# Optimization experiments

Measured on AMD Instinct MI355X. Metric: run time of the kernel, lower is better.

Reference implementation:

```python
import jax, jax.numpy as jnp
import numpy as np

EPS = 1e-6


def _mp_match(reps, att, kernel):
    """BiMPM multi-perspective match.
    reps: (B,L,D); att: (B,L,D) or (B,1,D); kernel: (M,D).
    Returns (B,L,1+M): [tanh(sum(reps*att)), tanh(sum_d reps*kernel_m*att)].
    """
    prod = reps * att                                   # (B,L,D)
    cos = jnp.tanh(jnp.sum(prod, axis=-1, keepdims=True))   # (B,L,1)
    mp = jnp.tanh(jnp.einsum('bld,md->blm', prod, kernel))  # (B,L,M)
    return jnp.concatenate([cos, mp], axis=-1)


def setup_inputs() -> dict:
    key = jax.random.key(0)
    ks = jax.random.split(key, 12)
    B, Llt, Lrt, D, M, A = 32, 128, 128, 512, 64, 128
    H = D // 2
    u = lambda k, shape: jax.random.uniform(k, shape, jnp.float32, -0.05, 0.05)  # keras 'uniform' init
    return {
        'reps_lt': jax.random.normal(ks[0], (B, Llt, D), jnp.float32),
        'h_lt_fw': jax.random.normal(ks[1], (B, H), jnp.float32),
        'h_lt_bw': jax.random.normal(ks[2], (B, H), jnp.float32),
        'reps_rt': jax.random.normal(ks[3], (B, Lrt, D), jnp.float32),
        'h_rt_fw': jax.random.normal(ks[4], (B, H), jnp.float32),
        'h_rt_bw': jax.random.normal(ks[5], (B, H), jnp.float32),
        'kernel_full': u(ks[6], (M, D)),
        'kernel_mpool': u(ks[7], (M, D)),
        'attn_w1': u(ks[8], (D, A)),
        'diag_w': u(ks[9], (A,)),
        'kernel_att': u(ks[10], (M, D)),
        'kernel_maxatt': u(ks[11], (M, D)),
    }


def reference(reps_lt, h_lt_fw, h_lt_bw, reps_rt, h_rt_fw, h_rt_bw,
              kernel_full, kernel_mpool, attn_w1, diag_w,
              kernel_att, kernel_maxatt):
    # ---- full match: each left timestep vs last BiLSTM state of right ----
    h_rt = jnp.concatenate([h_rt_fw, h_rt_bw], axis=-1)[:, None, :]  # (B,1,D)
    full = _mp_match(reps_lt, h_rt, kernel_full)                     # (B,Ll,1+M)

    # ---- max-pooling match ----
    # t[b,r,l,m] = tanh(sum_d R[b,r,d]*K[m,d]*L[b,l,d]); max over right positions r
    r_scaled = jnp.einsum('brd,md->brmd', reps_rt, kernel_mpool)     # (B,Lr,M,D)
    t = jnp.tanh(jnp.einsum('brmd,bld->brlm', r_scaled, reps_lt))    # (B,Lr,Ll,M)
    mpool = jnp.max(t, axis=1)                                       # (B,Ll,M)

    # ---- attentive match ----
    a_lt = jnp.tanh(reps_lt @ attn_w1) * diag_w                      # (B,Ll,A)
    a_rt = jnp.tanh(reps_rt @ attn_w1)                               # (B,Lr,A)
    scores = jnp.einsum('bla,bra->blr', a_lt, a_rt)                  # (B,Ll,Lr)
    probs = jax.nn.softmax(scores, axis=-1)
    att = jnp.einsum('blr,brd->bld', probs, reps_rt)                 # (B,Ll,D)
    attentive = _mp_match(reps_lt, att, kernel_att)                  # (B,Ll,1+M)

    # ---- max-attentive match ----
    num = jnp.einsum('bld,brd->blr', reps_lt, reps_rt)
    n_lt = jnp.sqrt(jnp.maximum(jnp.sum(reps_lt * reps_lt, -1), EPS))[:, :, None]
    n_rt = jnp.sqrt(jnp.maximum(jnp.sum(reps_rt * reps_rt, -1), EPS))[:, None, :]
    rel = num / n_rt / n_lt                                          # (B,Ll,Lr)
    idx = jnp.argmax(rel, axis=2)                                    # (B,Ll) int
    max_att = jnp.take_along_axis(reps_rt, idx[:, :, None], axis=1)  # (B,Ll,D)
    maxatt = _mp_match(reps_lt, max_att, kernel_maxatt)              # (B,Ll,1+M)

    return jnp.concatenate([full, mpool, attentive, maxatt], axis=-1)  # (B,Ll,3+4M)
```

## Files before the change

kernel.cpp:

```cpp
#include <hip/hip_runtime.h>
#include <hip/hip_bf16.h>
#include <math.h>
#include <stdint.h>

typedef __attribute__((ext_vector_type(8))) short short8;
typedef __attribute__((ext_vector_type(4))) float float4v;

#define DEV static __device__ __forceinline__

DEV float bflo(unsigned int u) { union { unsigned int i; float f; } v; v.i = u << 16; return v.f; }
DEV float bfhi(unsigned int u) { union { unsigned int i; float f; } v; v.i = u & 0xffff0000u; return v.f; }
DEV unsigned short f2bf(float f) {
    union { float f; unsigned int i; } v; v.f = f;
    unsigned int x = v.i;
    return (unsigned short)((x + 0x7fffu + ((x >> 16) & 1u)) >> 16);
}
DEV unsigned int pack2(float a, float b) { return (unsigned int)f2bf(a) | ((unsigned int)f2bf(b) << 16); }
#if __has_builtin(__builtin_amdgcn_cvt_pk_bf16_f32)
DEV unsigned int pack2_fast(float a, float b) {
    typedef __attribute__((ext_vector_type(2))) short short2v;
    short2v r = __builtin_amdgcn_cvt_pk_bf16_f32(a, b);
    union { short2v s; unsigned int u; } v; v.s = r; return v.u;
}
#else
DEV unsigned int pack2_fast(float a, float b) { return pack2(a, b); }
#endif
DEV void unpack8(uint4 u, float* f) {
    f[0]=bflo(u.x); f[1]=bfhi(u.x); f[2]=bflo(u.y); f[3]=bfhi(u.y);
    f[4]=bflo(u.z); f[5]=bfhi(u.z); f[6]=bflo(u.w); f[7]=bfhi(u.w);
}

DEV void async16(const unsigned short* g, unsigned short* l) {
    __builtin_amdgcn_global_load_lds(
        (const __attribute__((address_space(1))) unsigned int*)g,
        (__attribute__((address_space(3))) unsigned int*)l, 16, 0, 0);
}

__global__ __launch_bounds__(256) void prep_kernel(const float* __restrict__ lt,
                                                   const float* __restrict__ rt,
                                                   const float* __restrict__ kf,
                                                   const float* __restrict__ kmp,
                                                   const float* __restrict__ ka,
                                                   const float* __restrict__ km,
                                                   const float* __restrict__ w1,
                                                   unsigned short* __restrict__ ltb,
                                                   unsigned short* __restrict__ rtb,
                                                   unsigned short* __restrict__ kb,
                                                   unsigned short* __restrict__ w1t,
                                                   unsigned short* __restrict__ rtbT,
                                                   double* __restrict__ rsq) {
    __shared__ double ws2[2][2];
    __shared__ float tile[32][33];
    int bid = blockIdx.x, t = threadIdx.x;
    if (bid < 1024) {
        bool isRt = bid >= 512;
        int base = (isRt ? (bid - 512) : bid) * 8;
        int rl = t >> 7;
        int c  = t & 127;
        const float* srcb = isRt ? rt : lt;
        unsigned short* dstb = isRt ? rtb : ltb;
        #pragma unroll
        for (int p = 0; p < 4; ++p) {
            int row = base + p * 2 + rl;
            const float* src = srcb + (size_t)row * 512;
            float4 v = *(const float4*)(src + c * 4);
            ushort4 o;
            o.x = f2bf(v.x); o.y = f2bf(v.y); o.z = f2bf(v.z); o.w = f2bf(v.w);
            *(ushort4*)(dstb + (size_t)row * 512 + c * 4) = o;
            if (isRt) {
                double s = (double)v.x * v.x + (double)v.y * v.y
                         + (double)v.z * v.z + (double)v.w * v.w;
                #pragma unroll
                for (int off = 1; off < 64; off <<= 1) s += __shfl_xor(s, off, 64);
                if ((c & 63) == 0) ws2[rl][c >> 6] = s;
                __syncthreads();
                if (c == 0) rsq[row] = 1.0 / sqrt(ws2[rl][0] + ws2[rl][1]);
                __syncthreads();
            }
        }
    } else if (bid < 1152) {
        int kbk = bid - 1024;
        int ksel = kbk >> 5;
        const float* src = (ksel == 0) ? kf : (ksel == 1) ? kmp : (ksel == 2) ? ka : km;
        int off = (kbk & 31) * 1024 + t * 4;
        float4 v = *(const float4*)(src + off);
        ushort4 o;
        o.x = f2bf(v.x); o.y = f2bf(v.y); o.z = f2bf(v.z); o.w = f2bf(v.w);
        *(ushort4*)(kb + ksel * 32768 + off) = o;
    } else if (bid < 1216) {
        int b2 = bid - 1152;
        int d0 = (b2 & 15) * 32, a0 = (b2 >> 4) * 32;
        int r = t >> 5, c = t & 31;
        #pragma unroll
        for (int i = 0; i < 32; i += 8)
            tile[r + i][c] = w1[(size_t)(d0 + r + i) * 128 + a0 + c];
        __syncthreads();
        #pragma unroll
        for (int i = 0; i < 32; i += 8)
            w1t[(size_t)(a0 + r + i) * 512 + d0 + c] = f2bf(tile[c][r + i]);
    } else {
        int b3 = bid - 1216;
        int b = b3 >> 6;
        int tid = b3 & 63;
        int d0 = (tid & 15) * 32;
        int r0 = (tid >> 4) * 32;
        int r = t >> 5, c = t & 31;
        #pragma unroll
        for (int i = 0; i < 32; i += 8)
            tile[r + i][c] = rt[(size_t)(b * 128 + r0 + r + i) * 512 + d0 + c];
        __syncthreads();
        #pragma unroll
        for (int i = 0; i < 32; i += 8)
            rtbT[(size_t)(b * 512 + d0 + r + i) * 128 + r0 + c] = f2bf(tile[c][r + i]);
    }
}

__global__ __launch_bounds__(256, 3) void mid_kernel(
        const unsigned short* __restrict__ ltb,
        const unsigned short* __restrict__ rtb,
        const unsigned short* __restrict__ w1t,
        const float* __restrict__ diag,
        unsigned short* __restrict__ a_all,
        const double* __restrict__ rsq,
        unsigned int* __restrict__ candp) {
    __shared__ __align__(16) unsigned char smem[52224];
    int bx = blockIdx.x;
    int t = threadIdx.x;
    int wave = t >> 6, lane = t & 63;
    int q = lane >> 4, col = lane & 15, kq = q * 8;

    if (bx < 32) {
        int sb = bx;
        int xcd = sb & 7;
        int b = xcd * 4 + (sb >> 3);
        unsigned short* ltS = (unsigned short*)smem;
        unsigned short* rtL = (unsigned short*)(smem + 16384);
        float* rsqf = (float*)(smem + 49152);
        unsigned int (*candL)[2] = (unsigned int(*)[2])(smem + 49664);
        int wl = wave & 1, wr = wave >> 1;
        const unsigned short* ltp = ltb + (size_t)b * 65536;
        const unsigned short* rtp = rtb + (size_t)b * 65536;
        int srow = t >> 3, cg8 = t & 7, cg = cg8 * 8;
        int gsw = (cg8 ^ (srow & 7)) * 8;
        int wbase = (t & ~63) * 8;

        #pragma unroll
        for (int it = 0; it < 4; ++it)
            async16(rtp + (size_t)(it * 32 + srow) * 512 + gsw,
                    rtL + it * 2048 + wbase);
        uint4 plt[4];
        #pragma unroll
        for (int it = 0; it < 4; ++it)
            plt[it] = *(const uint4*)(ltp + (size_t)(it * 32 + srow) * 512 + cg);
        if (t < 128) rsqf[t] = (float)rsq[b * 128 + t];

        float4v acc[4][4] = {};
        for (int k0i = 0; k0i < 8; ++k0i) {
            #pragma unroll
            for (int it = 0; it < 4; ++it) {
                int row = it * 32 + srow;
                *(uint4*)&ltS[row * 64 + gsw] = plt[it];
            }
            __syncthreads();
            if (k0i < 7) {
                int k0n = (k0i + 1) * 64;
                int bofs = ((k0i + 1) & 1) * 8192;
                #pragma unroll
                for (int it = 0; it < 4; ++it)
                    async16(rtp + (size_t)(it * 32 + srow) * 512 + k0n + gsw,
                            rtL + bofs + it * 2048 + wbase);
                #pragma unroll
                for (int it = 0; it < 4; ++it)
                    plt[it] = *(const uint4*)(ltp + (size_t)(it * 32 + srow) * 512 + k0n + cg);
            }
            const unsigned short* rb = rtL + (k0i & 1) * 8192;
            #pragma unroll
            for (int kk = 0; kk < 64; kk += 32) {
                short8 af[4], bfr[4];
                #pragma unroll
                for (int i = 0; i < 4; ++i) {
                    int rowA = wl * 64 + i * 16 + col;
                    int slotA = ((kk >> 3) + q) ^ (rowA & 7);
                    af[i] = *(const short8*)&ltS[rowA * 64 + slotA * 8];
                }
                #pragma unroll
                for (int j = 0; j < 4; ++j) {
                    int row = wr * 64 + j * 16 + col;
                    int slot = ((kk >> 3) + q) ^ (row & 7);
                    bfr[j] = *(const short8*)&rb[row * 64 + slot * 8];
                }
                #pragma unroll
                for (int i = 0; i < 4; ++i)
                    #pragma unroll
                    for (int j = 0; j < 4; ++j)
                        acc[i][j] = __builtin_amdgcn_mfma_f32_16x16x32_bf16(af[i], bfr[j], acc[i][j], 0, 0, 0);
            }
            __syncthreads();
        }
        float rq[4];
        #pragma unroll
        for (int j = 0; j < 4; ++j) rq[j] = rsqf[wr * 64 + j * 16 + col];
        #pragma unroll
        for (int i = 0; i < 4; ++i)
            #pragma unroll
            for (int ii = 0; ii < 4; ++ii) {
                float v1 = -3.0e38f, v2 = -3.0e38f; int i1 = 0, i2 = 1;
                #pragma unroll
                for (int j = 0; j < 4; ++j) {
                    int rc = wr * 64 + j * 16 + col;
                    float s = acc[i][j][ii] * rq[j];
                    if (s > v1) { v2 = v1; i2 = i1; v1 = s; i1 = rc; }
                    else if (s > v2) { v2 = s; i2 = rc; }
                }
                #pragma unroll
                for (int off = 1; off < 16; off <<= 1) {
                    float u1 = __shfl_xor(v1, off, 64); int j1 = __shfl_xor(i1, off, 64);
                    float u2 = __shfl_xor(v2, off, 64); int j2 = __shfl_xor(i2, off, 64);
                    if (u1 > v1) {
                        float ov = v1; int oi = i1;
                        v1 = u1; i1 = j1;
                        if (u2 > ov) { v2 = u2; i2 = j2; } else { v2 = ov; i2 = oi; }
                    } else if (u1 > v2) { v2 = u1; i2 = j1; }
                }
                if (col == 0)
                    candL[wl * 64 + i * 16 + q * 4 + ii][wr] =
                        (unsigned int)i1 | ((unsigned int)i2 << 8);
            }
        __syncthreads();
        if (t < 128)
            candp[b * 128 + t] = candL[t][0] | (candL[t][1] << 16);

    } else {
        int R0 = (bx - 32) * 32;
        unsigned short (*aS)[72] = (unsigned short(*)[72])smem;
        unsigned short (*bS)[72] = (unsigned short(*)[72])(smem + 4608);
        float* diagS = (float*)(smem + 4608 + 18432);
        int wl = wave & 1, wr = wave >> 1;
        if (t < 128) diagS[t] = diag[t];
        const unsigned short* src = (R0 < 4096) ? (ltb + (size_t)R0 * 512) : (rtb + (size_t)(R0 - 4096) * 512);
        float4v acc[4] = {};
        for (int k0 = 0; k0 < 512; k0 += 64) {
            {
                int row = t >> 3, cg = (t & 7) * 8;
                *(uint4*)&aS[row][cg] = *(const uint4*)(src + (size_t)row * 512 + k0 + cg);
            }
            #pragma unroll
            for (int it = 0; it < 4; ++it) {
                int id = it * 256 + t;
                int row = id >> 3, cg = (id & 7) * 8;
                *(uint4*)&bS[row][cg] = *(const uint4*)(w1t + (size_t)row * 512 + k0 + cg);
            }
            __syncthreads();
            #pragma unroll
            for (int kk = 0; kk < 64; kk += 32) {
                short8 af = *(const short8*)&aS[wl * 16 + col][kk + kq];
                #pragma unroll
                for (int j = 0; j < 4; ++j) {
                    short8 bf = *(const short8*)&bS[wr * 64 + j * 16 + col][kk + kq];
                    acc[j] = __builtin_amdgcn_mfma_f32_16x16x32_bf16(af, bf, acc[j], 0, 0, 0);
                }
            }
            __syncthreads();
        }
        bool isLt = (R0 < 4096);
        #pragma unroll
        for (int j = 0; j < 4; ++j)
            #pragma unroll
            for (int ii = 0; ii < 4; ++ii) {
                int rowl = wl * 16 + q * 4 + ii;
                int n = wr * 64 + j * 16 + col;
                float v = tanhf(acc[j][ii]);
                if (isLt) v *= diagS[n];
                a_all[((size_t)(R0 + rowl)) * 128 + n] = f2bf(v);
            }
    }
}

__global__ __launch_bounds__(512, 4) void main_kernel(
        const unsigned short* __restrict__ ltb,
        const unsigned short* __restrict__ rtb,
        const unsigned short* __restrict__ kmb,
        const unsigned short* __restrict__ a_all,
        const unsigned short* __restrict__ rtbT,
        const float* __restrict__ ltf,
        const float* __restrict__ rtf,
        const double* __restrict__ rsq,
        const unsigned short* __restrict__ kb,
        const float* __restrict__ hfw,
        const float* __restrict__ hbw,
        const unsigned int* __restrict__ candp,
        float* __restrict__ out) {
    __shared__ __align__(16) unsigned char smem[81664];
    int bx = blockIdx.x;
    int t = threadIdx.x;
    int wave = t >> 6, lane = t & 63;
    int q = lane >> 4, col = lane & 15, kq = q * 8;

    int xcd = bx & 7;
    int s = bx >> 3;
    int g = s / 11;
    int r = s - g * 11;

    if (r < 8) {
        int lm = g * 8 + r;
        int b = xcd * 4 + (lm >> 6);
        int m = lm & 63;
        unsigned short* ltS = (unsigned short*)smem;
        unsigned short* rtL = (unsigned short*)(smem + 16384);
        float (*mx)[4] = (float(*)[4])(smem + 49152);
        int wl = wave & 1, wr = wave >> 1;
        const unsigned short* ltp = ltb + (size_t)b * 65536;
        const unsigned short* rtp = rtb + (size_t)b * 65536;
        const unsigned short* kr = kmb + (size_t)m * 512;
        int srow = t >> 3, cg8 = t & 7, cg = cg8 * 8;
        int gsw = (cg8 ^ (srow & 7)) * 8;

        #pragma unroll
        for (int it = 0; it < 2; ++it)
            async16(rtp + (size_t)(it * 64 + srow) * 512 + gsw,
                    rtL + it * 4096 + t * 8);
        uint4 pk = *(const uint4*)(kr + cg);
        uint4 plt[2];
        #pragma unroll
        for (int it = 0; it < 2; ++it)
            plt[it] = *(const uint4*)(ltp + (size_t)(it * 64 + srow) * 512 + cg);

        float4v acc[4][2] = {};
        for (int k0i = 0; k0i < 8; ++k0i) {
            float kf8[8]; unpack8(pk, kf8);
            #pragma unroll
            for (int it = 0; it < 2; ++it) {
                int row = it * 64 + srow;
                float lf[8]; unpack8(plt[it], lf);
                uint4 sv;
                sv.x = pack2_fast(lf[0] * kf8[0], lf[1] * kf8[1]);
                sv.y = pack2_fast(lf[2] * kf8[2], lf[3] * kf8[3]);
                sv.z = pack2_fast(lf[4] * kf8[4], lf[5] * kf8[5]);
                sv.w = pack2_fast(lf[6] * kf8[6], lf[7] * kf8[7]);
                *(uint4*)&ltS[row * 64 + gsw] = sv;
            }
            __syncthreads();
            if (k0i < 7) {
                int k0n = (k0i + 1) * 64;
                int bofs = ((k0i + 1) & 1) * 8192;
                #pragma unroll
                for (int it = 0; it < 2; ++it)
                    async16(rtp + (size_t)(it * 64 + srow) * 512 + k0n + gsw,
                            rtL + bofs + it * 4096 + t * 8);
                pk = *(const uint4*)(kr + k0n + cg);
                #pragma unroll
                for (int it = 0; it < 2; ++it)
                    plt[it] = *(const uint4*)(ltp + (size_t)(it * 64 + srow) * 512 + k0n + cg);
            }
            const unsigned short* rb = rtL + (k0i & 1) * 8192;
            #pragma unroll
            for (int kk = 0; kk < 64; kk += 32) {
                short8 af[4], bfr[2];
                #pragma unroll
                for (int i = 0; i < 4; ++i) {
                    int rowA = wl * 64 + i * 16 + col;
                    int slotA = ((kk >> 3) + q) ^ (rowA & 7);
                    af[i] = *(const short8*)&ltS[rowA * 64 + slotA * 8];
                }
                #pragma unroll
                for (int j = 0; j < 2; ++j) {
                    int row = wr * 32 + j * 16 + col;
                    int slot = ((kk >> 3) + q) ^ (row & 7);
                    bfr[j] = *(const short8*)&rb[row * 64 + slot * 8];
                }
                #pragma unroll
                for (int i = 0; i < 4; ++i)
                    #pragma unroll
                    for (int j = 0; j < 2; ++j)
                        acc[i][j] = __builtin_amdgcn_mfma_f32_16x16x32_bf16(af[i], bfr[j], acc[i][j], 0, 0, 0);
            }
            __syncthreads();
        }
        #pragma unroll
        for (int i = 0; i < 4; ++i)
            #pragma unroll
            for (int ii = 0; ii < 4; ++ii) {
                float v = fmaxf(acc[i][0][ii], acc[i][1][ii]);
                #pragma unroll
                for (int off = 1; off < 16; off <<= 1) v = fmaxf(v, __shfl_xor(v, off, 64));
                if (col == 0) mx[wl * 64 + i * 16 + q * 4 + ii][wr] = v;
            }
        __syncthreads();
        if (t < 128) {
            float v = fmaxf(fmaxf(mx[t][0], mx[t][1]), fmaxf(mx[t][2], mx[t][3]));
            out[((size_t)(b * 128 + t)) * 259 + 65 + m] = tanhf(v);
        }

    } else if (r == 8) {
        int la = g;
        int b = xcd * 4 + (la >> 3);
        int lg = la & 7;
        int L0 = lg * 16;
        unsigned short (*altS)[136]  = (unsigned short(*)[136])(smem);
        unsigned short (*artS)[136]  = (unsigned short(*)[136])(smem + 4352);
        unsigned short (*prodsF)[520]= (unsigned short(*)[520])(smem + 55552);
        float (*pmax)[8] = (float(*)[8])(smem + 80640);
        float (*psum)[8] = (float(*)[8])(smem + 81152);
        const unsigned short* kb_att = kb + 2 * 32768;

        if (t < 256) {
            int row = t >> 4, c0 = (t & 15) * 8;
            *(uint4*)&altS[row][c0] = *(const uint4*)(a_all + ((size_t)(b * 128 + L0 + row)) * 128 + c0);
        }
        {
            int row = t >> 2, c0 = (t & 3) * 32;
            const unsigned short* src = a_all + ((size_t)(4096 + b * 128 + row)) * 128 + c0;
            #pragma unroll
            for (int i = 0; i < 4; ++i)
                *(uint4*)&artS[row][c0 + i * 8] = *(const uint4*)(src + i * 8);
        }
        __syncthreads();

        float4v acc = {};
        #pragma unroll
        for (int kk = 0; kk < 128; kk += 32) {
            short8 af = *(const short8*)&altS[col][kk + kq];
            short8 bf = *(const short8*)&artS[wave * 16 + col][kk + kq];
            acc = __builtin_amdgcn_mfma_f32_16x16x32_bf16(af, bf, acc, 0, 0, 0);
        }
        float m4[4], p4[4];
        #pragma unroll
        for (int ii = 0; ii < 4; ++ii) {
            float v = acc[ii];
            #pragma unroll
            for (int off = 1; off < 16; off <<= 1) v = fmaxf(v, __shfl_xor(v, off, 64));
            m4[ii] = v;
        }
        if (col == 0) {
            #pragma unroll
            for (int ii = 0; ii < 4; ++ii) pmax[q * 4 + ii][wave] = m4[ii];
        }
        __syncthreads();
        #pragma unroll
        for (int ii = 0; ii < 4; ++ii) {
            float M = pmax[q * 4 + ii][0];
            #pragma unroll
            for (int w = 1; w < 8; ++w) M = fmaxf(M, pmax[q * 4 + ii][w]);
            p4[ii] = expf(acc[ii] - M);
            float sv = p4[ii];
            #pragma unroll
            for (int off = 1; off < 16; off <<= 1) sv += __shfl_xor(sv, off, 64);
            m4[ii] = sv;
        }
        if (col == 0) {
            #pragma unroll
            for (int ii = 0; ii < 4; ++ii) psum[q * 4 + ii][wave] = m4[ii];
        }
        __syncthreads();
        unsigned short* Pb = (unsigned short*)smem;
        #pragma unroll
        for (int ii = 0; ii < 4; ++ii) {
            float S = psum[q * 4 + ii][0] + psum[q * 4 + ii][1] + psum[q * 4 + ii][2] + psum[q * 4 + ii][3]
                    + psum[q * 4 + ii][4] + psum[q * 4 + ii][5] + psum[q * 4 + ii][6] + psum[q * 4 + ii][7];
            Pb[(q * 4 + ii) * 136 + wave * 16 + col] = f2bf(p4[ii] / S);
        }

        unsigned short* Bc = (unsigned short*)(smem + 4352);
        float* attF = (float*)(smem + 39168);
        const unsigned short* rtT = rtbT + (size_t)b * 65536;
        for (int cc = 0; cc < 4; ++cc) {
            #pragma unroll
            for (int i = 0; i < 4; ++i) {
                int rid = i * 32 + (t >> 4);
                int d   = (rid >> 4) * 64 + cc * 16 + (rid & 15);
                int sg  = (t & 15) ^ (rid & 15);
                async16(rtT + (size_t)d * 128 + sg * 8, Bc + i * 4096 + t * 8);
            }
            __syncthreads();
            float4v pacc = {};
            #pragma unroll
            for (int ks = 0; ks < 4; ++ks) {
                short8 afP = *(const short8*)&Pb[col * 136 + ks * 32 + kq];
                short8 bfB = *(const short8*)&Bc[(wave * 16 + col) * 128 + (((ks * 4 + q) ^ col) * 8)];
                pacc = __builtin_amdgcn_mfma_f32_16x16x32_bf16(afP, bfB, pacc, 0, 0, 0);
            }
            #pragma unroll
            for (int ii = 0; ii < 4; ++ii)
                attF[(q * 4 + ii) * 512 + wave * 64 + cc * 16 + col] = pacc[ii];
            __syncthreads();
        }

        int l = t >> 5, cd = t & 31;
        float a8[2][8];
        #pragma unroll
        for (int pass = 0; pass < 2; ++pass) {
            *(float4*)&a8[pass][0] = *(const float4*)&attF[l * 512 + pass * 256 + cd * 8];
            *(float4*)&a8[pass][4] = *(const float4*)&attF[l * 512 + pass * 256 + cd * 8 + 4];
        }
        __syncthreads();

        int grow = b * 128 + L0 + l;
        const float* ltrow = ltf + (size_t)grow * 512;
        float csum = 0.f;
        #pragma unroll
        for (int pass = 0; pass < 2; ++pass) {
            int d0 = pass * 256 + cd * 8;
            float lf[8];
            *(float4*)&lf[0] = *(const float4*)(ltrow + d0);
            *(float4*)&lf[4] = *(const float4*)(ltrow + d0 + 4);
            float pf[8];
            #pragma unroll
            for (int k = 0; k < 8; ++k) { pf[k] = lf[k] * a8[pass][k]; csum += pf[k]; }
            uint4 o;
            o.x = pack2(pf[0], pf[1]); o.y = pack2(pf[2], pf[3]);
            o.z = pack2(pf[4], pf[5]); o.w = pack2(pf[6], pf[7]);
            *(uint4*)&prodsF[l][d0] = o;
        }
        #pragma unroll
        for (int off = 1; off < 32; off <<= 1) csum += __shfl_xor(csum, off, 64);
        if (cd == 0) out[(size_t)grow * 259 + 129] = tanhf(csum);

        unsigned short* Ks = &artS[0][0];
        float* red = (float*)(smem + 39168);
        for (int half = 0; half < 2; ++half) {
            __syncthreads();
            {
                int row = t >> 4, c0 = (t & 15) * 32;
                const unsigned short* src = kb_att + ((size_t)(half * 32 + row)) * 512 + c0;
                #pragma unroll
                for (int i = 0; i < 4; ++i)
                    *(uint4*)&Ks[row * 520 + c0 + i * 8] = *(const uint4*)(src + i * 8);
            }
            __syncthreads();
            float4v pacc[2] = {};
            #pragma unroll
            for (int kk = 0; kk < 64; kk += 32) {
                short8 af = *(const short8*)&prodsF[col][wave * 64 + kk + kq];
                #pragma unroll
                for (int j = 0; j < 2; ++j) {
                    short8 bf = *(const short8*)&Ks[(j * 16 + col) * 520 + wave * 64 + kk + kq];
                    pacc[j] = __builtin_amdgcn_mfma_f32_16x16x32_bf16(af, bf, pacc[j], 0, 0, 0);
                }
            }
            #pragma unroll
            for (int j = 0; j < 2; ++j)
                #pragma unroll
                for (int ii = 0; ii < 4; ++ii)
                    red[((wave * 2 + j) * 16 + q * 4 + ii) * 16 + col] = pacc[j][ii];
            __syncthreads();
            {
                int ll = t >> 5, jm = t & 31;
                int j = jm >> 4, mc = jm & 15;
                float sv = 0.f;
                #pragma unroll
                for (int w = 0; w < 8; ++w) sv += red[((w * 2 + j) * 16 + ll) * 16 + mc];
                out[((size_t)(b * 128 + L0 + ll)) * 259 + 130 + half * 32 + jm] = tanhf(sv);
            }
        }

    } else {
        int lb = g * 2 + (r - 9);
        int mode = (lb >> 5) ? 2 : 0;
        int b = xcd * 4 + ((lb >> 3) & 3);
        int lg = lb & 7;
        int L0 = lg * 16;
        unsigned short (*prods)[520] = (unsigned short(*)[520])smem;
        unsigned short* Ks = (unsigned short*)(smem + 16640);
        float* red = (float*)(smem + 49920);
        double* dvs2 = (double*)(smem + 66304);
        int* idxl = (int*)(smem + 66816);
        const unsigned short* Kp = kb + (size_t)((mode == 0) ? 0 : 3 * 32768);
        int obase = (mode == 0) ? 0 : 194;

        if (mode == 2) {
            int dotid = t >> 3, sub = t & 7;
            int l = dotid >> 2, c = dotid & 3;
            unsigned int cpl = candp[b * 128 + L0 + l];
            int rr0 = (cpl >> (c * 8)) & 0xff;
            const float* lrow = ltf + ((size_t)(b * 128 + L0 + l)) * 512;
            const float* rrow = rtf + ((size_t)(b * 128 + rr0)) * 512;
            double sv = 0.0;
            #pragma unroll 8
            for (int k = 0; k < 64; ++k) {
                int d = sub * 64 + k;
                sv = fma((double)lrow[d], (double)rrow[d], sv);
            }
            #pragma unroll
            for (int off = 1; off < 8; off <<= 1) sv += __shfl_xor(sv, off, 64);
            if (sub == 0) dvs2[dotid] = sv * rsq[b * 128 + rr0];
            __syncthreads();
            if (t < 16) {
                unsigned int cl = candp[b * 128 + L0 + t];
                int bi = 256; double bv = -1.0e300;
                #pragma unroll
                for (int cc = 0; cc < 4; ++cc) {
                    int rr = (cl >> (cc * 8)) & 0xff;
                    double v = dvs2[t * 4 + cc];
                    if (v > bv || (v == bv && rr < bi)) { bv = v; bi = rr; }
                }
                idxl[t] = bi;
            }
            __syncthreads();
        }

        if (t < 256) {
            int l = t >> 4, c = t & 15;
            int grow = b * 128 + L0 + l;
            const float* ltrow = ltf + (size_t)grow * 512;
            const unsigned short* avrow = 0;
            if (mode == 2) avrow = rtb + ((size_t)(b * 128 + idxl[l])) * 512;
            float csum = 0.f;
            #pragma unroll
            for (int pass = 0; pass < 4; ++pass) {
                int d0 = pass * 128 + c * 8;
                float lf[8], af[8], pf[8];
                *(float4*)&lf[0] = *(const float4*)(ltrow + d0);
                *(float4*)&lf[4] = *(const float4*)(ltrow + d0 + 4);
                if (mode == 0) {
                    const float* h = (d0 < 256) ? (hfw + b * 256 + d0) : (hbw + b * 256 + d0 - 256);
                    *(float4*)&af[0] = *(const float4*)h;
                    *(float4*)&af[4] = *(const float4*)(h + 4);
                } else {
                    uint4 av = *(const uint4*)(avrow + d0);
                    unpack8(av, af);
                }
                #pragma unroll
                for (int k = 0; k < 8; ++k) { pf[k] = lf[k] * af[k]; csum += pf[k]; }
                uint4 o;
                o.x = pack2(pf[0], pf[1]); o.y = pack2(pf[2], pf[3]);
                o.z = pack2(pf[4], pf[5]); o.w = pack2(pf[6], pf[7]);
                *(uint4*)&prods[l][d0] = o;
            }
            #pragma unroll
            for (int off = 1; off < 16; off <<= 1) csum += __shfl_xor(csum, off, 64);
            if (c == 0) out[(size_t)grow * 259 + obase] = tanhf(csum);
        }
        for (int half = 0; half < 2; ++half) {
            {
                int row = t >> 4, c0 = (t & 15) * 32;
                const unsigned short* src = Kp + ((size_t)(half * 32 + row)) * 512 + c0;
                #pragma unroll
                for (int i = 0; i < 4; ++i)
                    *(uint4*)&Ks[row * 520 + c0 + i * 8] = *(const uint4*)(src + i * 8);
            }
            __syncthreads();
            float4v acc2[2] = {};
            #pragma unroll
            for (int kk = 0; kk < 64; kk += 32) {
                short8 af = *(const short8*)&prods[col][wave * 64 + kk + kq];
                #pragma unroll
                for (int j = 0; j < 2; ++j) {
                    short8 bf = *(const short8*)&Ks[(j * 16 + col) * 520 + wave * 64 + kk + kq];
                    acc2[j] = __builtin_amdgcn_mfma_f32_16x16x32_bf16(af, bf, acc2[j], 0, 0, 0);
                }
            }
            #pragma unroll
            for (int j = 0; j < 2; ++j)
                #pragma unroll
                for (int ii = 0; ii < 4; ++ii)
                    red[((wave * 2 + j) * 16 + q * 4 + ii) * 16 + col] = acc2[j][ii];
            __syncthreads();
            {
                int ll = t >> 5, jm = t & 31;
                int j = jm >> 4, mc = jm & 15;
                float sv = 0.f;
                #pragma unroll
                for (int w = 0; w < 8; ++w) sv += red[((w * 2 + j) * 16 + ll) * 16 + mc];
                out[((size_t)(b * 128 + L0 + ll)) * 259 + obase + 1 + half * 32 + jm] = tanhf(sv);
            }
            __syncthreads();
        }
    }
}

extern "C" void kernel_launch(void* const* d_in, const int* in_sizes, int n_in,
                              void* d_out, int out_size, void* d_ws, size_t ws_size,
                              hipStream_t stream) {
    const float* lt  = (const float*)d_in[0];
    const float* rt  = (const float*)d_in[3];
    const float* hfw = (const float*)d_in[4];
    const float* hbw = (const float*)d_in[5];
    const float* kf  = (const float*)d_in[6];
    const float* kmp = (const float*)d_in[7];
    const float* w1  = (const float*)d_in[8];
    const float* dia = (const float*)d_in[9];
    const float* ka  = (const float*)d_in[10];
    const float* km  = (const float*)d_in[11];
    float* out = (float*)d_out;

    char* wsb = (char*)d_ws;
    unsigned short* ltb16 = (unsigned short*)(wsb);
    unsigned short* rtb16 = (unsigned short*)(wsb + 4194304);
    unsigned short* kb16  = (unsigned short*)(wsb + 8388608);
    unsigned short* w1t   = (unsigned short*)(wsb + 8650752);
    unsigned short* a_all = (unsigned short*)(wsb + 8781824);
    unsigned short* rtbT  = (unsigned short*)(wsb + 10878976);
    double*         rsq   = (double*)(wsb + 15073280);
    unsigned int*   candp = (unsigned int*)(wsb + 15106048);

    prep_kernel<<<3264, 256, 0, stream>>>(lt, rt, kf, kmp, ka, km, w1, ltb16, rtb16, kb16, w1t, rtbT, rsq);
    mid_kernel<<<288, 256, 0, stream>>>(ltb16, rtb16, w1t, dia, a_all, rsq, candp);
    main_kernel<<<2816, 512, 0, stream>>>(ltb16, rtb16, kb16 + 32768, a_all, rtbT,
                                          lt, rt, rsq, kb16, hfw, hbw, candp, out);
}
```

Measured before the change: 198.8 us.

## Merge prep and mid kernels, converting fp32 inputs to bf16 inline

Folds the mid kernel's work (max-attentive argmax candidate search and the attention projection tanh(X·W1)) into the prep kernel launch as extra blocks. These blocks now read fp32 inputs directly and convert to bf16 on the fly, instead of waiting for prep's bf16 copies. The right-side norms are computed inline in fp32, and W1 is read transposed straight from global memory, so the w1t transpose disappears. This removes one kernel launch and the serialization between prep and mid. The cost is more global traffic: fp32 loads, and uncoalesced strided W1 reads inside the MFMA loop. The candidate search also loses its async-load double buffering and now uses an fp32 norm where it used a double one.

New measurement: 195.0 us. About the same (-1.9%).

```diff
diff --git a/kernel.cpp b/kernel.cpp
--- a/kernel.cpp
+++ b/kernel.cpp
@@ -43,137 +43,64 @@
                                                    const float* __restrict__ ka,
                                                    const float* __restrict__ km,
                                                    const float* __restrict__ w1,
+                                                   const float* __restrict__ diag,
                                                    unsigned short* __restrict__ ltb,
                                                    unsigned short* __restrict__ rtb,
                                                    unsigned short* __restrict__ kb,
-                                                   unsigned short* __restrict__ w1t,
                                                    unsigned short* __restrict__ rtbT,
-                                                   double* __restrict__ rsq) {
-    __shared__ double ws2[2][2];
-    __shared__ float tile[32][33];
+                                                   double* __restrict__ rsq,
+                                                   unsigned short* __restrict__ a_all,
+                                                   unsigned int* __restrict__ candp) {
+    __shared__ __align__(16) unsigned char smem[34304];
     int bid = blockIdx.x, t = threadIdx.x;
-    if (bid < 1024) {
-        bool isRt = bid >= 512;
-        int base = (isRt ? (bid - 512) : bid) * 8;
-        int rl = t >> 7;
-        int c  = t & 127;
-        const float* srcb = isRt ? rt : lt;
-        unsigned short* dstb = isRt ? rtb : ltb;
-        #pragma unroll
-        for (int p = 0; p < 4; ++p) {
-            int row = base + p * 2 + rl;
-            const float* src = srcb + (size_t)row * 512;
-            float4 v = *(const float4*)(src + c * 4);
-            ushort4 o;
-            o.x = f2bf(v.x); o.y = f2bf(v.y); o.z = f2bf(v.z); o.w = f2bf(v.w);
-            *(ushort4*)(dstb + (size_t)row * 512 + c * 4) = o;
-            if (isRt) {
-                double s = (double)v.x * v.x + (double)v.y * v.y
-                         + (double)v.z * v.z + (double)v.w * v.w;
-                #pragma unroll
-                for (int off = 1; off < 64; off <<= 1) s += __shfl_xor(s, off, 64);
-                if ((c & 63) == 0) ws2[rl][c >> 6] = s;
-                __syncthreads();
-                if (c == 0) rsq[row] = 1.0 / sqrt(ws2[rl][0] + ws2[rl][1]);
-                __syncthreads();
-            }
-        }
-    } else if (bid < 1152) {
-        int kbk = bid - 1024;
-        int ksel = kbk >> 5;
-        const float* src = (ksel == 0) ? kf : (ksel == 1) ? kmp : (ksel == 2) ? ka : km;
-        int off = (kbk & 31) * 1024 + t * 4;
-        float4 v = *(const float4*)(src + off);
-        ushort4 o;
-        o.x = f2bf(v.x); o.y = f2bf(v.y); o.z = f2bf(v.z); o.w = f2bf(v.w);
-        *(ushort4*)(kb + ksel * 32768 + off) = o;
-    } else if (bid < 1216) {
-        int b2 = bid - 1152;
-        int d0 = (b2 & 15) * 32, a0 = (b2 >> 4) * 32;
-        int r = t >> 5, c = t & 31;
-        #pragma unroll
-        for (int i = 0; i < 32; i += 8)
-            tile[r + i][c] = w1[(size_t)(d0 + r + i) * 128 + a0 + c];
-        __syncthreads();
-        #pragma unroll
-        for (int i = 0; i < 32; i += 8)
-            w1t[(size_t)(a0 + r + i) * 512 + d0 + c] = f2bf(tile[c][r + i]);
-    } else {
-        int b3 = bid - 1216;
-        int b = b3 >> 6;
-        int tid = b3 & 63;
-        int d0 = (tid & 15) * 32;
-        int r0 = (tid >> 4) * 32;
-        int r = t >> 5, c = t & 31;
-        #pragma unroll
-        for (int i = 0; i < 32; i += 8)
-            tile[r + i][c] = rt[(size_t)(b * 128 + r0 + r + i) * 512 + d0 + c];
-        __syncthreads();
-        #pragma unroll
-        for (int i = 0; i < 32; i += 8)
-            rtbT[(size_t)(b * 512 + d0 + r + i) * 128 + r0 + c] = f2bf(tile[c][r + i]);
-    }
-}
-
-__global__ __launch_bounds__(256, 3) void mid_kernel(
-        const unsigned short* __restrict__ ltb,
-        const unsigned short* __restrict__ rtb,
-        const unsigned short* __restrict__ w1t,
-        const float* __restrict__ diag,
-        unsigned short* __restrict__ a_all,
-        const double* __restrict__ rsq,
-        unsigned int* __restrict__ candp) {
-    __shared__ __align__(16) unsigned char smem[52224];
-    int bx = blockIdx.x;
-    int t = threadIdx.x;
     int wave = t >> 6, lane = t & 63;
     int q = lane >> 4, col = lane & 15, kq = q * 8;
 
-    if (bx < 32) {
-        int sb = bx;
-        int xcd = sb & 7;
-        int b = xcd * 4 + (sb >> 3);
+    if (bid < 32) {
+        int xcd = bid & 7;
+        int b = xcd * 4 + (bid >> 3);
         unsigned short* ltS = (unsigned short*)smem;
-        unsigned short* rtL = (unsigned short*)(smem + 16384);
-        float* rsqf = (float*)(smem + 49152);
-        unsigned int (*candL)[2] = (unsigned int(*)[2])(smem + 49664);
+        unsigned short* rtS = (unsigned short*)(smem + 16384);
+        float* rnorm = (float*)(smem + 32768);
+        unsigned int (*candL)[2] = (unsigned int(*)[2])(smem + 33280);
         int wl = wave & 1, wr = wave >> 1;
-        const unsigned short* ltp = ltb + (size_t)b * 65536;
-        const unsigned short* rtp = rtb + (size_t)b * 65536;
+        const float* ltF = lt + (size_t)b * 65536;
+        const float* rtF = rt + (size_t)b * 65536;
         int srow = t >> 3, cg8 = t & 7, cg = cg8 * 8;
-        int gsw = (cg8 ^ (srow & 7)) * 8;
-        int wbase = (t & ~63) * 8;
-
-        #pragma unroll
-        for (int it = 0; it < 4; ++it)
-            async16(rtp + (size_t)(it * 32 + srow) * 512 + gsw,
-                    rtL + it * 2048 + wbase);
-        uint4 plt[4];
-        #pragma unroll
-        for (int it = 0; it < 4; ++it)
-            plt[it] = *(const uint4*)(ltp + (size_t)(it * 32 + srow) * 512 + cg);
-        if (t < 128) rsqf[t] = (float)rsq[b * 128 + t];
+        if (t < 128) rnorm[t] = 0.f;
+        __syncthreads();
 
         float4v acc[4][4] = {};
         for (int k0i = 0; k0i < 8; ++k0i) {
+            int k0 = k0i * 64;
+            float rp[4];
             #pragma unroll
             for (int it = 0; it < 4; ++it) {
                 int row = it * 32 + srow;
-                *(uint4*)&ltS[row * 64 + gsw] = plt[it];
-            }
-            __syncthreads();
-            if (k0i < 7) {
-                int k0n = (k0i + 1) * 64;
-                int bofs = ((k0i + 1) & 1) * 8192;
-                #pragma unroll
-                for (int it = 0; it < 4; ++it)
-                    async16(rtp + (size_t)(it * 32 + srow) * 512 + k0n + gsw,
-                            rtL + bofs + it * 2048 + wbase);
-                #pragma unroll
-                for (int it = 0; it < 4; ++it)
-                    plt[it] = *(const uint4*)(ltp + (size_t)(it * 32 + srow) * 512 + k0n + cg);
-            }
-            const unsigned short* rb = rtL + (k0i & 1) * 8192;
+                int slot8 = (cg8 ^ (srow & 7)) * 8;
+                float4 a0 = *(const float4*)(ltF + (size_t)row * 512 + k0 + cg);
+                float4 a1 = *(const float4*)(ltF + (size_t)row * 512 + k0 + cg + 4);
+                uint4 s;
+                s.x = pack2_fast(a0.x, a0.y); s.y = pack2_fast(a0.z, a0.w);
+                s.z = pack2_fast(a1.x, a1.y); s.w = pack2_fast(a1.z, a1.w);
+                *(uint4*)&ltS[row * 64 + slot8] = s;
+                float4 b0 = *(const float4*)(rtF + (size_t)row * 512 + k0 + cg);
+                float4 b1 = *(const float4*)(rtF + (size_t)row * 512 + k0 + cg + 4);
+                uint4 r;
+                r.x = pack2_fast(b0.x, b0.y); r.y = pack2_fast(b0.z, b0.w);
+                r.z = pack2_fast(b1.x, b1.y); r.w = pack2_fast(b1.z, b1.w);
+                *(uint4*)&rtS[row * 64 + slot8] = r;
+                rp[it] = b0.x * b0.x + b0.y * b0.y + b0.z * b0.z + b0.w * b0.w
+                       + b1.x * b1.x + b1.y * b1.y + b1.z * b1.z + b1.w * b1.w;
+            }
+            #pragma unroll
+            for (int off = 1; off < 8; off <<= 1)
+                #pragma unroll
+                for (int it = 0; it < 4; ++it) rp[it] += __shfl_xor(rp[it], off, 64);
+            if (cg8 == 0)
+                #pragma unroll
+                for (int it = 0; it < 4; ++it) rnorm[it * 32 + srow] += rp[it];
+            __syncthreads();
             #pragma unroll
             for (int kk = 0; kk < 64; kk += 32) {
                 short8 af[4], bfr[4];
@@ -187,7 +114,7 @@
                 for (int j = 0; j < 4; ++j) {
                     int row = wr * 64 + j * 16 + col;
                     int slot = ((kk >> 3) + q) ^ (row & 7);
-                    bfr[j] = *(const short8*)&rb[row * 64 + slot * 8];
+                    bfr[j] = *(const short8*)&rtS[row * 64 + slot * 8];
                 }
                 #pragma unroll
                 for (int i = 0; i < 4; ++i)
@@ -199,7 +126,10 @@
         }
         float rq[4];
         #pragma unroll
-        for (int j = 0; j < 4; ++j) rq[j] = rsqf[wr * 64 + j * 16 + col];
+        for (int j = 0; j < 4; ++j) {
+            float sN = rnorm[wr * 64 + j * 16 + col];
+            rq[j] = 1.0f / sqrtf(fmaxf(sN, 1e-6f));
+        }
         #pragma unroll
         for (int i = 0; i < 4; ++i)
             #pragma unroll
@@ -230,25 +160,24 @@
         if (t < 128)
             candp[b * 128 + t] = candL[t][0] | (candL[t][1] << 16);
 
-    } else {
-        int R0 = (bx - 32) * 32;
+    } else if (bid < 288) {
+        int R0 = (bid - 32) * 32;
         unsigned short (*aS)[72] = (unsigned short(*)[72])smem;
-        unsigned short (*bS)[72] = (unsigned short(*)[72])(smem + 4608);
-        float* diagS = (float*)(smem + 4608 + 18432);
+        float* diagS = (float*)(smem + 4608);
         int wl = wave & 1, wr = wave >> 1;
         if (t < 128) diagS[t] = diag[t];
-        const unsigned short* src = (R0 < 4096) ? (ltb + (size_t)R0 * 512) : (rtb + (size_t)(R0 - 4096) * 512);
+        const float* srcf = (R0 < 4096) ? (lt + (size_t)R0 * 512)
+                                        : (rt + (size_t)(R0 - 4096) * 512);
         float4v acc[4] = {};
         for (int k0 = 0; k0 < 512; k0 += 64) {
             {
                 int row = t >> 3, cg = (t & 7) * 8;
-                *(uint4*)&aS[row][cg] = *(const uint4*)(src + (size_t)row * 512 + k0 + cg);
-            }
-            #pragma unroll
-            for (int it = 0; it < 4; ++it) {
-                int id = it * 256 + t;
-                int row = id >> 3, cg = (id & 7) * 8;
-                *(uint4*)&bS[row][cg] = *(const uint4*)(w1t + (size_t)row * 512 + k0 + cg);
+                float4 f0 = *(const float4*)(srcf + (size_t)row * 512 + k0 + cg);
+                float4 f1 = *(const float4*)(srcf + (size_t)row * 512 + k0 + cg + 4);
+                uint4 s;
+                s.x = pack2_fast(f0.x, f0.y); s.y = pack2_fast(f0.z, f0.w);
+                s.z = pack2_fast(f1.x, f1.y); s.w = pack2_fast(f1.z, f1.w);
+                *(uint4*)&aS[row][cg] = s;
             }
             __syncthreads();
             #pragma unroll
@@ -256,7 +185,14 @@
                 short8 af = *(const short8*)&aS[wl * 16 + col][kk + kq];
                 #pragma unroll
                 for (int j = 0; j < 4; ++j) {
-                    short8 bf = *(const short8*)&bS[wr * 64 + j * 16 + col][kk + kq];
+                    int n = wr * 64 + j * 16 + col;
+                    const float* wp = w1 + (size_t)(k0 + kk + kq) * 128 + n;
+                    float b0 = wp[0],     b1 = wp[128],   b2 = wp[256],   b3 = wp[384];
+                    float b4 = wp[512],   b5 = wp[640],   b6 = wp[768],   b7 = wp[896];
+                    uint4 s;
+                    s.x = pack2_fast(b0, b1); s.y = pack2_fast(b2, b3);
+                    s.z = pack2_fast(b4, b5); s.w = pack2_fast(b6, b7);
+                    short8 bf = *(short8*)&s;
                     acc[j] = __builtin_amdgcn_mfma_f32_16x16x32_bf16(af, bf, acc[j], 0, 0, 0);
                 }
             }
@@ -273,6 +209,61 @@
                 if (isLt) v *= diagS[n];
                 a_all[((size_t)(R0 + rowl)) * 128 + n] = f2bf(v);
             }
+
+    } else {
+        int pb = bid - 288;
+        if (pb < 1024) {
+            double (*ws2)[2] = (double(*)[2])smem;
+            bool isRt = pb >= 512;
+            int base = (isRt ? (pb - 512) : pb) * 8;
+            int rl = t >> 7;
+            int c  = t & 127;
+            const float* srcb = isRt ? rt : lt;
+            unsigned short* dstb = isRt ? rtb : ltb;
+            #pragma unroll
+            for (int p = 0; p < 4; ++p) {
+                int row = base + p * 2 + rl;
+                const float* src = srcb + (size_t)row * 512;
+                float4 v = *(const float4*)(src + c * 4);
+                ushort4 o;
+                o.x = f2bf(v.x); o.y = f2bf(v.y); o.z = f2bf(v.z); o.w = f2bf(v.w);
+                *(ushort4*)(dstb + (size_t)row * 512 + c * 4) = o;
+                if (isRt) {
+                    double s = (double)v.x * v.x + (double)v.y * v.y
+                             + (double)v.z * v.z + (double)v.w * v.w;
+                    #pragma unroll
+                    for (int off = 1; off < 64; off <<= 1) s += __shfl_xor(s, off, 64);
+                    if ((c & 63) == 0) ws2[rl][c >> 6] = s;
+                    __syncthreads();
+                    if (c == 0) rsq[row] = 1.0 / sqrt(ws2[rl][0] + ws2[rl][1]);
+                    __syncthreads();
+                }
+            }
+        } else if (pb < 1152) {
+            int kbk = pb - 1024;
+            int ksel = kbk >> 5;
+            const float* src = (ksel == 0) ? kf : (ksel == 1) ? kmp : (ksel == 2) ? ka : km;
+            int off = (kbk & 31) * 1024 + t * 4;
+            float4 v = *(const float4*)(src + off);
+            ushort4 o;
+            o.x = f2bf(v.x); o.y = f2bf(v.y); o.z = f2bf(v.z); o.w = f2bf(v.w);
+            *(ushort4*)(kb + ksel * 32768 + off) = o;
+        } else {
+            float (*tile)[33] = (float(*)[33])smem;
+            int b3 = pb - 1152;
+            int b = b3 >> 6;
+            int tid = b3 & 63;
+            int d0 = (tid & 15) * 32;
+            int r0 = (tid >> 4) * 32;
+            int r = t >> 5, c = t & 31;
+            #pragma unroll
+            for (int i = 0; i < 32; i += 8)
+                tile[r + i][c] = rt[(size_t)(b * 128 + r0 + r + i) * 512 + d0 + c];
+            __syncthreads();
+            #pragma unroll
+            for (int i = 0; i < 32; i += 8)
+                rtbT[(size_t)(b * 512 + d0 + r + i) * 128 + r0 + c] = f2bf(tile[c][r + i]);
+        }
     }
 }
 
@@ -687,14 +678,13 @@
     unsigned short* ltb16 = (unsigned short*)(wsb);
     unsigned short* rtb16 = (unsigned short*)(wsb + 4194304);
     unsigned short* kb16  = (unsigned short*)(wsb + 8388608);
-    unsigned short* w1t   = (unsigned short*)(wsb + 8650752);
     unsigned short* a_all = (unsigned short*)(wsb + 8781824);
     unsigned short* rtbT  = (unsigned short*)(wsb + 10878976);
     double*         rsq   = (double*)(wsb + 15073280);
     unsigned int*   candp = (unsigned int*)(wsb + 15106048);
 
-    prep_kernel<<<3264, 256, 0, stream>>>(lt, rt, kf, kmp, ka, km, w1, ltb16, rtb16, kb16, w1t, rtbT, rsq);
-    mid_kernel<<<288, 256, 0, stream>>>(ltb16, rtb16, w1t, dia, a_all, rsq, candp);
+    prep_kernel<<<3488, 256, 0, stream>>>(lt, rt, kf, kmp, ka, km, w1, dia,
+                                          ltb16, rtb16, kb16, rtbT, rsq, a_all, candp);
     main_kernel<<<2816, 512, 0, stream>>>(ltb16, rtb16, kb16 + 32768, a_all, rtbT,
                                           lt, rt, rsq, kb16, hfw, hbw, candp, out);
 }
```
